# Optimization experiments

Hardware: AMD Instinct MI355X
Metric: run time of the kernel (lower is better)

The kernel has to match this reference:

```python
import jax, jax.numpy as jnp
import numpy as np

HID = 128  # hardcoded in the original module (hyperparameters['hidden_sizes'])
BETA1, BETA2, ADAM_EPS = 0.9, 0.999, 1e-8  # torch.optim.Adam defaults


def _xavier(k, shape):
    lim = np.sqrt(6.0 / (shape[0] + shape[1]))
    return jax.random.uniform(k, shape, jnp.float32, -lim, lim)


def setup_inputs() -> dict:
    key = jax.random.key(0)
    k0, k1, k2 = jax.random.split(key, 3)
    input_size, output_size = 65536, 4096
    return {
        "x": jax.random.uniform(k0, (input_size,), jnp.float32),
        "W1": _xavier(k1, (input_size, HID)),
        "W2": _xavier(k2, (HID, output_size)),
        "b_in": jnp.zeros((input_size,), jnp.float32),
        "b_h": jnp.zeros((HID,), jnp.float32),
        "b_out": jnp.zeros((output_size,), jnp.float32),
        "hidden0": jnp.zeros((HID,), jnp.float32),
        "output0": jnp.zeros((output_size,), jnp.float32),
        "n_iterations": 256,
        "epsilon": 0.01,
    }


def _drho(s):
    # gradient mask of rho = clamp(s, 0, 1), matching torch clamp backward
    return ((s >= 0.0) & (s <= 1.0)).astype(s.dtype)


def reference(x, W1, W2, b_in, b_h, b_out, hidden0, output0, n_iterations, epsilon):
    r_x = jnp.clip(x, 0.0, 1.0)
    xW1 = r_x @ W1  # [HID], constant across iterations (input is clamped/fixed)

    def adam(p, g, m, v, t1):
        m = BETA1 * m + (1.0 - BETA1) * g
        v = BETA2 * v + (1.0 - BETA2) * g * g
        mhat = m / (1.0 - jnp.power(BETA1, t1))
        vhat = v / (1.0 - jnp.power(BETA2, t1))
        return p - epsilon * mhat / (jnp.sqrt(vhat) + ADAM_EPS), m, v

    def step(carry, t):
        h, o, mh, vh, mo, vo = carry
        r_h = jnp.clip(h, 0.0, 1.0)
        r_o = jnp.clip(o, 0.0, 1.0)
        # analytic dE/dh, dE/do of the quadratic Hopfield energy
        g_h = _drho(h) * (r_h - b_h - xW1 - W2 @ r_o)      # [HID]
        g_o = _drho(o) * (r_o - b_out - r_h @ W2)          # [output_size]
        t1 = t + 1.0
        h, mh, vh = adam(h, g_h, mh, vh, t1)
        o, mo, vo = adam(o, g_o, mo, vo, t1)
        return (h, o, mh, vh, mo, vo), None

    init = (hidden0, output0,
            jnp.zeros_like(hidden0), jnp.zeros_like(hidden0),
            jnp.zeros_like(output0), jnp.zeros_like(output0))
    (h, o, *_), _ = jax.lax.scan(step, init, jnp.arange(n_iterations, dtype=jnp.float32))
    return o
```

## Files before the change

kernel.cpp:

```cpp
#include <hip/hip_runtime.h>
#include <stdint.h>

#define HID   128
#define OUT   4096
#define NWG   8
#define SLICE 512
#define NT    512
#define NXB   128
#define RPX   512
#define NSLOT 4

typedef unsigned long long u64;
typedef unsigned int v2u __attribute__((ext_vector_type(2)));

__device__ __forceinline__ u64 pk(uint32_t tag, float v) {
  return ((u64)tag << 32) | (u64)__float_as_uint(v);
}

__device__ __forceinline__ float plane32_fold(float a, float b) {
  const v2u r = __builtin_amdgcn_permlane32_swap(__float_as_uint(a), __float_as_uint(b),
                                                 false, false);
  return __uint_as_float(r.x) + __uint_as_float(r.y);
}
__device__ __forceinline__ float dpp_ror8(float x) {
  return __int_as_float(
      __builtin_amdgcn_update_dpp(0, __float_as_int(x), 0x128, 0xF, 0xF, true));
}
__device__ __forceinline__ float dpp_add_xor2(float x) {
  const int y = __builtin_amdgcn_update_dpp(0, __float_as_int(x), 0x4E, 0xF, 0xF, true);
  return x + __int_as_float(y);
}
__device__ __forceinline__ float dpp_add_xor1(float x) {
  const int y = __builtin_amdgcn_update_dpp(0, __float_as_int(x), 0xB1, 0xF, 0xF, true);
  return x + __int_as_float(y);
}

__device__ __forceinline__ void bar_lgkm() {
  __builtin_amdgcn_sched_barrier(0);
  asm volatile("s_waitcnt lgkmcnt(0)" ::: "memory");
  __builtin_amdgcn_s_barrier();
  __builtin_amdgcn_sched_barrier(0);
}

__global__ __launch_bounds__(NT, 1) void k_all(
    const float* __restrict__ x,
    const float* __restrict__ W1,
    const float* __restrict__ W2,
    const float* __restrict__ b_h,
    const float* __restrict__ b_out,
    const float* __restrict__ h0,
    const float* __restrict__ o0,
    const int* __restrict__ n_iter_p,
    const float* __restrict__ eps_p,
    u64* __restrict__ pbuf,
    u64* __restrict__ xw1p,
    float* __restrict__ out) {

  __shared__ __attribute__((aligned(16))) float red[8 * SLICE];
  __shared__ __attribute__((aligned(16))) float rh_s[HID];
  __shared__ __attribute__((aligned(16))) float ro_s[SLICE];

  const int t = threadIdx.x;

  if (blockIdx.x >= NWG) {
    const int b = blockIdx.x - NWG;
    const int c4 = (t & 31) * 4;
    const int rseg = t >> 5;
    const int r0 = b * RPX + rseg * 32;
    float4 acc = make_float4(0.f, 0.f, 0.f, 0.f);
#pragma unroll 8
    for (int k = 0; k < 32; ++k) {
      const int r = r0 + k;
      const float rx = fminf(fmaxf(x[r], 0.f), 1.f);
      const float4 wv = *(const float4*)&W1[(size_t)r * HID + c4];
      acc.x = fmaf(rx, wv.x, acc.x); acc.y = fmaf(rx, wv.y, acc.y);
      acc.z = fmaf(rx, wv.z, acc.z); acc.w = fmaf(rx, wv.w, acc.w);
    }
    *(float4*)&red[rseg * HID + c4] = acc;
    __syncthreads();
    if (t < HID) {
      float s = 0.f;
#pragma unroll
      for (int k = 0; k < 16; k += 4)
        s += (red[k*HID + t] + red[(k+1)*HID + t]) + (red[(k+2)*HID + t] + red[(k+3)*HID + t]);
      __hip_atomic_store(&xw1p[b * HID + t], pk(1u, s),
                         __ATOMIC_RELAXED, __HIP_MEMORY_SCOPE_AGENT);
    }
    return;
  }

  const int wg = blockIdx.x;
  const int cg = t & 63;
  const int rg = t >> 6;
  const int n_iter = *n_iter_p;
  const float eps  = *eps_p;

  float w2[16][8];
  {
    const float* wp = W2 + (size_t)(rg * 16) * OUT + wg * SLICE + cg;
#pragma unroll
    for (int r = 0; r < 16; ++r)
#pragma unroll
      for (int k = 0; k < 8; ++k)
        w2[r][k] = wp[(size_t)r * OUT + 64 * k];
  }
#pragma unroll
  for (int r = 0; r < 16; ++r)
    asm volatile("" : "+v"(w2[r][0]), "+v"(w2[r][1]), "+v"(w2[r][2]), "+v"(w2[r][3]),
                      "+v"(w2[r][4]), "+v"(w2[r][5]), "+v"(w2[r][6]), "+v"(w2[r][7]));

  float bhx = 0.f, hh = 0.f, mh = 0.f, vh = 0.f;
  if (t < HID) {
    float s = 0.f;
#pragma unroll 1
    for (int ch = 0; ch < 8; ++ch) {
      u64 v[16];
      for (;;) {
#pragma unroll
        for (int k = 0; k < 16; ++k)
          v[k] = __hip_atomic_load(&xw1p[(ch * 16 + k) * HID + t],
                                   __ATOMIC_RELAXED, __HIP_MEMORY_SCOPE_AGENT);
        uint32_t bad = 0u;
#pragma unroll
        for (int k = 0; k < 16; ++k) bad |= ((uint32_t)(v[k] >> 32)) ^ 1u;
        if (bad == 0u) break;
        __builtin_amdgcn_s_sleep(2);
      }
#pragma unroll
      for (int k = 0; k < 16; ++k) s += __uint_as_float((uint32_t)v[k]);
    }
    bhx = b_h[t] + s;
    hh  = h0[t];
    rh_s[t] = fminf(fmaxf(hh, 0.f), 1.f);
  }
  float oo = o0[wg * SLICE + t];
  float mo = 0.f, vo = 0.f;
  const float bo = b_out[wg * SLICE + t];
  ro_s[t] = fminf(fmaxf(oo, 0.f), 1.f);
  __syncthreads();

  float bp1 = 1.f, bp2 = 1.f;
  u64 pref[8] = {0, 0, 0, 0, 0, 0, 0, 0};

  for (int it = 0; it < n_iter; ++it) {
    float aB[16];
    {
      float rov[8];
#pragma unroll
      for (int k = 0; k < 8; ++k) rov[k] = ro_s[cg + 64 * k];
#pragma unroll
      for (int r = 0; r < 16; ++r) {
        float a = w2[r][0] * rov[0];
#pragma unroll
        for (int k = 1; k < 8; ++k) a = fmaf(w2[r][k], rov[k], a);
        aB[r] = a;
      }
    }
    {
#pragma unroll
      for (int r = 0; r < 8; ++r)
        aB[r] = plane32_fold(aB[r], aB[r + 8]);
#pragma unroll
      for (int r = 0; r < 4; ++r) {
        const float keep = (cg & 16) ? aB[r + 4] : aB[r];
        const float send = (cg & 16) ? aB[r]     : aB[r + 4];
        aB[r] = keep + __shfl_xor(send, 16, 64);
      }
#pragma unroll
      for (int r = 0; r < 2; ++r) {
        const float keep = (cg & 8) ? aB[r + 2] : aB[r];
        const float send = (cg & 8) ? aB[r]     : aB[r + 2];
        aB[r] = keep + dpp_ror8(send);
      }
      {
        const float keep = (cg & 4) ? aB[1] : aB[0];
        const float send = (cg & 4) ? aB[0] : aB[1];
        aB[0] = keep + __shfl_xor(send, 4, 64);
      }
      aB[0] = dpp_add_xor2(aB[0]);
      aB[0] = dpp_add_xor1(aB[0]);
    }

    if (t < HID && it > 0) {
      const uint32_t tagc = (uint32_t)it;
      u64 v[8];
#pragma unroll
      for (int wi = 0; wi < 8; ++wi) v[wi] = pref[wi];
      uint32_t bad = 0u;
#pragma unroll
      for (int wi = 0; wi < 8; ++wi) bad |= ((uint32_t)(v[wi] >> 32)) ^ tagc;
      if (bad != 0u) {
        u64* pc = pbuf + (size_t)((it - 1) & (NSLOT - 1)) * (NWG * HID);
        do {
#pragma unroll
          for (int wi = 0; wi < 8; ++wi)
            v[wi] = __hip_atomic_load(&pc[wi * HID + t],
                                      __ATOMIC_RELAXED, __HIP_MEMORY_SCOPE_AGENT);
          bad = 0u;
#pragma unroll
          for (int wi = 0; wi < 8; ++wi) bad |= ((uint32_t)(v[wi] >> 32)) ^ tagc;
          if (bad != 0u) __builtin_amdgcn_s_sleep(1);
        } while (bad != 0u);
      }
      const float gsum = ((__uint_as_float((uint32_t)v[0]) + __uint_as_float((uint32_t)v[1]))
                        + (__uint_as_float((uint32_t)v[2]) + __uint_as_float((uint32_t)v[3])))
                       + ((__uint_as_float((uint32_t)v[4]) + __uint_as_float((uint32_t)v[5]))
                        + (__uint_as_float((uint32_t)v[6]) + __uint_as_float((uint32_t)v[7])));
      const float c1h = 1.f / (1.f - bp1);
      const float c2h = 1.f / (1.f - bp2);
      const float rh_old = fminf(fmaxf(hh, 0.f), 1.f);
      const float g = (hh >= 0.f && hh <= 1.f) ? (rh_old - bhx - gsum) : 0.f;
      mh = 0.9f * mh + 0.1f * g;
      vh = 0.999f * vh + 0.001f * g * g;
      hh -= eps * (mh * c1h) / (sqrtf(vh * c2h) + 1e-8f);
      rh_s[t] = fminf(fmaxf(hh, 0.f), 1.f);
    }

    if ((cg & 3) == 0) {
      u64* pp = pbuf + (size_t)(it & (NSLOT - 1)) * (NWG * HID)
                     + wg * HID + rg * 16 + (cg >> 2);
      __hip_atomic_store(pp, pk((uint32_t)(it + 1), aB[0]),
                         __ATOMIC_RELAXED, __HIP_MEMORY_SCOPE_AGENT);
    }

    bp1 *= 0.9f; bp2 *= 0.999f;
    const float c1 = 1.f / (1.f - bp1);
    const float c2 = 1.f / (1.f - bp2);

    bar_lgkm();

    {
      float aA[8] = {0.f, 0.f, 0.f, 0.f, 0.f, 0.f, 0.f, 0.f};
#pragma unroll
      for (int r = 0; r < 16; ++r) {
        const float rh = rh_s[rg * 16 + r];
#pragma unroll
        for (int k = 0; k < 8; ++k) aA[k] = fmaf(w2[r][k], rh, aA[k]);
      }
#pragma unroll
      for (int k = 0; k < 8; ++k)
        red[rg * SLICE + cg + 64 * k] = aA[k];
    }
    bar_lgkm();

    {
      const float s = ((red[t] + red[SLICE + t]) + (red[2*SLICE + t] + red[3*SLICE + t]))
                    + ((red[4*SLICE + t] + red[5*SLICE + t]) + (red[6*SLICE + t] + red[7*SLICE + t]));
      const float ro_old = fminf(fmaxf(oo, 0.f), 1.f);
      const float g = (oo >= 0.f && oo <= 1.f) ? (ro_old - bo - s) : 0.f;
      mo = 0.9f * mo + 0.1f * g;
      vo = 0.999f * vo + 0.001f * g * g;
      oo -= eps * (mo * c1) / (sqrtf(vo * c2) + 1e-8f);
      ro_s[t] = fminf(fmaxf(oo, 0.f), 1.f);
    }

    if (t < HID && it + 1 < n_iter) {
      const u64* pn = pbuf + (size_t)(it & (NSLOT - 1)) * (NWG * HID);
#pragma unroll
      for (int wi = 0; wi < 8; ++wi)
        pref[wi] = __hip_atomic_load(&pn[wi * HID + t],
                                     __ATOMIC_RELAXED, __HIP_MEMORY_SCOPE_AGENT);
    }

    bar_lgkm();
  }

  out[wg * SLICE + t] = oo;
}

extern "C" void kernel_launch(void* const* d_in, const int* in_sizes, int n_in,
                              void* d_out, int out_size, void* d_ws, size_t ws_size,
                              hipStream_t stream) {
  const float* x     = (const float*)d_in[0];
  const float* W1    = (const float*)d_in[1];
  const float* W2    = (const float*)d_in[2];
  const float* b_h   = (const float*)d_in[4];
  const float* b_out = (const float*)d_in[5];
  const float* h0    = (const float*)d_in[6];
  const float* o0    = (const float*)d_in[7];
  const int*   nit   = (const int*)d_in[8];
  const float* eps   = (const float*)d_in[9];

  u64*   pbuf = (u64*)d_ws;
  u64*   xw1p = (u64*)((char*)d_ws + 32768);
  float* out  = (float*)d_out;

  k_all<<<dim3(NWG + NXB), dim3(NT), 0, stream>>>(x, W1, W2, b_h, b_out, h0, o0,
                                                  nit, eps, pbuf, xw1p, out);
}
```

Measured before the change: 508.8 us.

## Split recurrent loop across 16 workgroups with 256-column output slices

Doubles the number of persistent workgroups for the iterative Adam loop and halves each one's output slice, so every thread holds half as many W2 registers and does half the FMAs per iteration. The cross-workgroup partial-sum exchange grows from 8 to 16 tagged entries per hidden unit, and the workspace offset is moved to make room. Half the threads now sit idle in the output update, and the larger exchange adds polling and reduction latency to the serial per-iteration critical path.

```diff
diff --git a/kernel.cpp b/kernel.cpp
--- a/kernel.cpp
+++ b/kernel.cpp
@@ -3,8 +3,8 @@
 
 #define HID   128
 #define OUT   4096
-#define NWG   8
-#define SLICE 512
+#define NWG   16
+#define SLICE 256
 #define NT    512
 #define NXB   128
 #define RPX   512
@@ -95,19 +95,18 @@
   const int n_iter = *n_iter_p;
   const float eps  = *eps_p;
 
-  float w2[16][8];
+  float w2[16][4];
   {
     const float* wp = W2 + (size_t)(rg * 16) * OUT + wg * SLICE + cg;
 #pragma unroll
     for (int r = 0; r < 16; ++r)
 #pragma unroll
-      for (int k = 0; k < 8; ++k)
+      for (int k = 0; k < 4; ++k)
         w2[r][k] = wp[(size_t)r * OUT + 64 * k];
   }
 #pragma unroll
   for (int r = 0; r < 16; ++r)
-    asm volatile("" : "+v"(w2[r][0]), "+v"(w2[r][1]), "+v"(w2[r][2]), "+v"(w2[r][3]),
-                      "+v"(w2[r][4]), "+v"(w2[r][5]), "+v"(w2[r][6]), "+v"(w2[r][7]));
+    asm volatile("" : "+v"(w2[r][0]), "+v"(w2[r][1]), "+v"(w2[r][2]), "+v"(w2[r][3]));
 
   float bhx = 0.f, hh = 0.f, mh = 0.f, vh = 0.f;
   if (t < HID) {
@@ -133,26 +132,30 @@
     hh  = h0[t];
     rh_s[t] = fminf(fmaxf(hh, 0.f), 1.f);
   }
-  float oo = o0[wg * SLICE + t];
-  float mo = 0.f, vo = 0.f;
-  const float bo = b_out[wg * SLICE + t];
-  ro_s[t] = fminf(fmaxf(oo, 0.f), 1.f);
+  float oo = 0.f, mo = 0.f, vo = 0.f, bo = 0.f;
+  if (t < SLICE) {
+    oo = o0[wg * SLICE + t];
+    bo = b_out[wg * SLICE + t];
+    ro_s[t] = fminf(fmaxf(oo, 0.f), 1.f);
+  }
   __syncthreads();
 
   float bp1 = 1.f, bp2 = 1.f;
-  u64 pref[8] = {0, 0, 0, 0, 0, 0, 0, 0};
+  u64 pref[16];
+#pragma unroll
+  for (int wi = 0; wi < 16; ++wi) pref[wi] = 0;
 
   for (int it = 0; it < n_iter; ++it) {
     float aB[16];
     {
-      float rov[8];
-#pragma unroll
-      for (int k = 0; k < 8; ++k) rov[k] = ro_s[cg + 64 * k];
+      float rov[4];
+#pragma unroll
+      for (int k = 0; k < 4; ++k) rov[k] = ro_s[cg + 64 * k];
 #pragma unroll
       for (int r = 0; r < 16; ++r) {
         float a = w2[r][0] * rov[0];
 #pragma unroll
-        for (int k = 1; k < 8; ++k) a = fmaf(w2[r][k], rov[k], a);
+        for (int k = 1; k < 4; ++k) a = fmaf(w2[r][k], rov[k], a);
         aB[r] = a;
       }
     }
@@ -183,29 +186,32 @@
 
     if (t < HID && it > 0) {
       const uint32_t tagc = (uint32_t)it;
-      u64 v[8];
-#pragma unroll
-      for (int wi = 0; wi < 8; ++wi) v[wi] = pref[wi];
+      u64 v[16];
+#pragma unroll
+      for (int wi = 0; wi < 16; ++wi) v[wi] = pref[wi];
       uint32_t bad = 0u;
 #pragma unroll
-      for (int wi = 0; wi < 8; ++wi) bad |= ((uint32_t)(v[wi] >> 32)) ^ tagc;
+      for (int wi = 0; wi < 16; ++wi) bad |= ((uint32_t)(v[wi] >> 32)) ^ tagc;
       if (bad != 0u) {
         u64* pc = pbuf + (size_t)((it - 1) & (NSLOT - 1)) * (NWG * HID);
         do {
 #pragma unroll
-          for (int wi = 0; wi < 8; ++wi)
+          for (int wi = 0; wi < 16; ++wi)
             v[wi] = __hip_atomic_load(&pc[wi * HID + t],
                                       __ATOMIC_RELAXED, __HIP_MEMORY_SCOPE_AGENT);
           bad = 0u;
 #pragma unroll
-          for (int wi = 0; wi < 8; ++wi) bad |= ((uint32_t)(v[wi] >> 32)) ^ tagc;
+          for (int wi = 0; wi < 16; ++wi) bad |= ((uint32_t)(v[wi] >> 32)) ^ tagc;
           if (bad != 0u) __builtin_amdgcn_s_sleep(1);
         } while (bad != 0u);
       }
-      const float gsum = ((__uint_as_float((uint32_t)v[0]) + __uint_as_float((uint32_t)v[1]))
-                        + (__uint_as_float((uint32_t)v[2]) + __uint_as_float((uint32_t)v[3])))
-                       + ((__uint_as_float((uint32_t)v[4]) + __uint_as_float((uint32_t)v[5]))
-                        + (__uint_as_float((uint32_t)v[6]) + __uint_as_float((uint32_t)v[7])));
+      float gv[16];
+#pragma unroll
+      for (int wi = 0; wi < 16; ++wi) gv[wi] = __uint_as_float((uint32_t)v[wi]);
+      const float gsum = (((gv[0] + gv[1]) + (gv[2] + gv[3]))
+                        + ((gv[4] + gv[5]) + (gv[6] + gv[7])))
+                       + (((gv[8] + gv[9]) + (gv[10] + gv[11]))
+                        + ((gv[12] + gv[13]) + (gv[14] + gv[15])));
       const float c1h = 1.f / (1.f - bp1);
       const float c2h = 1.f / (1.f - bp2);
       const float rh_old = fminf(fmaxf(hh, 0.f), 1.f);
@@ -230,20 +236,20 @@
     bar_lgkm();
 
     {
-      float aA[8] = {0.f, 0.f, 0.f, 0.f, 0.f, 0.f, 0.f, 0.f};
+      float aA[4] = {0.f, 0.f, 0.f, 0.f};
 #pragma unroll
       for (int r = 0; r < 16; ++r) {
         const float rh = rh_s[rg * 16 + r];
 #pragma unroll
-        for (int k = 0; k < 8; ++k) aA[k] = fmaf(w2[r][k], rh, aA[k]);
-      }
-#pragma unroll
-      for (int k = 0; k < 8; ++k)
+        for (int k = 0; k < 4; ++k) aA[k] = fmaf(w2[r][k], rh, aA[k]);
+      }
+#pragma unroll
+      for (int k = 0; k < 4; ++k)
         red[rg * SLICE + cg + 64 * k] = aA[k];
     }
     bar_lgkm();
 
-    {
+    if (t < SLICE) {
       const float s = ((red[t] + red[SLICE + t]) + (red[2*SLICE + t] + red[3*SLICE + t]))
                     + ((red[4*SLICE + t] + red[5*SLICE + t]) + (red[6*SLICE + t] + red[7*SLICE + t]));
       const float ro_old = fminf(fmaxf(oo, 0.f), 1.f);
@@ -257,7 +263,7 @@
     if (t < HID && it + 1 < n_iter) {
       const u64* pn = pbuf + (size_t)(it & (NSLOT - 1)) * (NWG * HID);
 #pragma unroll
-      for (int wi = 0; wi < 8; ++wi)
+      for (int wi = 0; wi < 16; ++wi)
         pref[wi] = __hip_atomic_load(&pn[wi * HID + t],
                                      __ATOMIC_RELAXED, __HIP_MEMORY_SCOPE_AGENT);
     }
@@ -265,7 +271,7 @@
     bar_lgkm();
   }
 
-  out[wg * SLICE + t] = oo;
+  if (t < SLICE) out[wg * SLICE + t] = oo;
 }
 
 extern "C" void kernel_launch(void* const* d_in, const int* in_sizes, int n_in,
@@ -282,7 +288,7 @@
   const float* eps   = (const float*)d_in[9];
 
   u64*   pbuf = (u64*)d_ws;
-  u64*   xw1p = (u64*)((char*)d_ws + 32768);
+  u64*   xw1p = (u64*)((char*)d_ws + 65536);
   float* out  = (float*)d_out;
 
   k_all<<<dim3(NWG + NXB), dim3(NT), 0, stream>>>(x, W1, W2, b_h, b_out, h0, o0,
```

Measured after the change: 500.6 us. About the same (-1.6%).
